# Kernel tuning notes

Hardware: AMD Instinct MI355X
Metric: run time of the kernel (lower is better)

The kernel has to match this reference:

```python
import jax, jax.numpy as jnp
import numpy as np

B, S, D = 4, 1024, 2048
N_HEADS, N_KV_HEADS = 32, 8
HEAD_DIM = D // N_HEADS          # 64
HALF = HEAD_DIM // 2             # 32
N_REP = N_HEADS // N_KV_HEADS    # 4


def setup_inputs() -> dict:
    key = jax.random.key(0)
    ks = jax.random.split(key, 6)
    # rotary tables: freqs_cis = exp(i * t * theta^( -2j/d )), real cos/sin halves
    inv_freq = 1.0 / (10000.0 ** (np.arange(0, HEAD_DIM, 2, dtype=np.float32) / HEAD_DIM))
    t = np.arange(S, dtype=np.float32)
    angles = np.outer(t, inv_freq)  # [S, HALF]
    return {
        "x": jax.random.normal(ks[0], (B, S, D), dtype=jnp.float32),
        "pos_cos": jnp.asarray(np.cos(angles), dtype=jnp.float32),
        "pos_sin": jnp.asarray(np.sin(angles), dtype=jnp.float32),
        "wq": jax.random.normal(ks[1], (D, N_HEADS * HEAD_DIM), dtype=jnp.float32) / np.sqrt(D),
        "wk": jax.random.normal(ks[2], (D, N_KV_HEADS * HEAD_DIM), dtype=jnp.float32) / np.sqrt(D),
        "wv": jax.random.normal(ks[3], (D, N_KV_HEADS * HEAD_DIM), dtype=jnp.float32) / np.sqrt(D),
        "wo": jax.random.normal(ks[4], (D, D), dtype=jnp.float32) / np.sqrt(D),
    }


def _apply_rotary(t, cos, sin):
    # t: [B, S, H, head_dim]; pairs of consecutive elements form complex numbers
    te = t[..., 0::2]  # real parts  [B,S,H,HALF]
    to = t[..., 1::2]  # imag parts
    c = cos[None, :, None, :]
    s = sin[None, :, None, :]
    re = te * c - to * s
    im = te * s + to * c
    return jnp.stack([re, im], axis=-1).reshape(t.shape)


def reference(x, pos_cos, pos_sin, wq, wk, wv, wo):
    b, s, d = x.shape
    xq = (x @ wq).reshape(b, s, N_HEADS, HEAD_DIM)
    xk = (x @ wk).reshape(b, s, N_KV_HEADS, HEAD_DIM)
    xv = (x @ wv).reshape(b, s, N_KV_HEADS, HEAD_DIM)
    xq = _apply_rotary(xq, pos_cos, pos_sin)
    xk = _apply_rotary(xk, pos_cos, pos_sin)
    # GQA: repeat kv heads (kv head h -> heads h*N_REP..h*N_REP+N_REP-1)
    xk = jnp.repeat(xk, N_REP, axis=2)
    xv = jnp.repeat(xv, N_REP, axis=2)
    scores = jnp.einsum("bqhd,bkhd->bhqk", xq, xk) / np.sqrt(HEAD_DIM).astype(np.float32)
    causal = jnp.triu(jnp.ones((s, s), dtype=bool), k=1)
    scores = jnp.where(causal[None, None], jnp.float32(-jnp.inf), scores)
    attn = jax.nn.softmax(scores.astype(jnp.float32), axis=-1).astype(x.dtype)
    out = jnp.einsum("bhqk,bkhd->bqhd", attn, xv).reshape(b, s, d)
    return out @ wo
```

## Files before the change

kernel.cpp:

```cpp
#include <hip/hip_runtime.h>
#include <hip/hip_bf16.h>


typedef __bf16 bf16x8 __attribute__((ext_vector_type(8)));
typedef float  f32x4  __attribute__((ext_vector_type(4)));

#define DEV static __device__ __forceinline__

DEV unsigned short f2bf(float f) {
  __hip_bfloat16 h = __float2bfloat16(f);
  unsigned short u;
  __builtin_memcpy(&u, &h, 2);
  return u;
}
DEV float bf2f(unsigned short u) {
  unsigned int ui = ((unsigned int)u) << 16;
  float f;
  __builtin_memcpy(&f, &ui, 4);
  return f;
}

typedef const unsigned int __attribute__((address_space(1)))* as1_u32cp;
typedef unsigned int __attribute__((address_space(3)))* as3_u32p;

DEV void load16_lds(const unsigned short* g, unsigned short* l) {
  __builtin_amdgcn_global_load_lds((as1_u32cp)(unsigned long long)g,
                                   (as3_u32p)(unsigned int)(unsigned long long)l,
                                   16, 0, 0);
}

DEV f32x4 mfma16x16(bf16x8 a, bf16x8 b, f32x4 c) {
  return __builtin_amdgcn_mfma_f32_16x16x32_bf16(a, b, c, 0, 0, 0);
}

__global__ __launch_bounds__(256) void k_convert_x(const float* __restrict__ x,
                                                   unsigned short* __restrict__ xb, int n) {
  int i = (blockIdx.x * 256 + threadIdx.x) * 4;
  if (i < n) {
    float4 v = *(const float4*)(x + i);
    ushort4 o;
    o.x = f2bf(v.x); o.y = f2bf(v.y); o.z = f2bf(v.z); o.w = f2bf(v.w);
    *(ushort4*)(xb + i) = o;
  }
}

__global__ __launch_bounds__(256) void k_transpose_w(const float* __restrict__ src,
                                                     unsigned short* __restrict__ dst, int N) {
  __shared__ float t[32][33];
  const int n0 = blockIdx.x * 32, k0 = blockIdx.y * 32;
  const int tx = threadIdx.x & 31, ty = threadIdx.x >> 5;
#pragma unroll
  for (int i = 0; i < 4; i++) {
    int k = k0 + ty + i * 8;
    t[ty + i * 8][tx] = src[(size_t)k * N + n0 + tx];
  }
  __syncthreads();
#pragma unroll
  for (int i = 0; i < 4; i++) {
    int n = n0 + ty + i * 8;
    dst[(size_t)n * 2048 + k0 + tx] = f2bf(t[tx][ty + i * 8]);
  }
}


DEV bf16x8 ldfrag(const unsigned short* base, int row, int colslot) {
  return *(const bf16x8*)&base[row * 64 + (((colslot) ^ (row & 7)) << 3)];
}

template <int OUTF32>
__global__ __launch_bounds__(512) void k_gemm8(const unsigned short* __restrict__ A,
                                               const unsigned short* __restrict__ Bt,
                                               void* __restrict__ Cp, int M, int N, int K) {
  __shared__ __align__(16) unsigned short As[2][16384];
  __shared__ __align__(16) unsigned short Bs[2][16384];
  const int nbx = N >> 8;
  const int nwg = gridDim.x;
  int wg = blockIdx.x;
  wg = (wg & 7) * (nwg >> 3) + (wg >> 3);
  const int bx = wg % nbx, by = wg / nbx;
  const int m0 = by << 8, n0 = bx << 8;
  const int tid = threadIdx.x;
  const int lane = tid & 63, wid = tid >> 6;
  const int wm = wid >> 2, wn = wid & 3;
  const int l15 = lane & 15, kg = lane >> 4;
  const int NT = K >> 6;

  const int rl = tid >> 3;
  const int gcol = (((tid & 7) ^ (rl & 7)) << 3);
  const unsigned short* Ag = &A[(size_t)(m0 + rl) * K + gcol];
  const unsigned short* Bg = &Bt[(size_t)(n0 + rl) * K + gcol];
  const int ldsb = wid * 8 * 64;

#define STAGE_TILE(buf, kt)                                                        \
  {                                                                                \
    const int _k0 = (kt) << 6;                                                     \
    _Pragma("unroll") for (int i = 0; i < 4; i++)                                  \
        load16_lds(&Ag[(size_t)(i * 64) * K + _k0], &As[buf][i * 64 * 64 + ldsb]); \
    _Pragma("unroll") for (int i = 0; i < 4; i++)                                  \
        load16_lds(&Bg[(size_t)(i * 64) * K + _k0], &Bs[buf][i * 64 * 64 + ldsb]); \
  }

  f32x4 acc[8][4] = {};

  STAGE_TILE(0, 0)
  STAGE_TILE(1, 1)
  asm volatile("s_waitcnt vmcnt(8)" ::: "memory");
  __builtin_amdgcn_s_barrier();

  for (int t = 0; t < NT; t++) {
    const unsigned short* at = As[t & 1];
    const unsigned short* bt = Bs[t & 1];
    bf16x8 af[4][2], bfr[2][2];

#pragma unroll
    for (int fm = 0; fm < 4; fm++)
#pragma unroll
      for (int kc = 0; kc < 2; kc++)
        af[fm][kc] = ldfrag(at, wm * 128 + fm * 16 + l15, kc * 4 + kg);
#pragma unroll
    for (int fn = 0; fn < 2; fn++)
#pragma unroll
      for (int kc = 0; kc < 2; kc++)
        bfr[fn][kc] = ldfrag(bt, wn * 64 + fn * 16 + l15, kc * 4 + kg);
    __builtin_amdgcn_s_barrier();
    __builtin_amdgcn_s_setprio(1);
#pragma unroll
    for (int fm = 0; fm < 4; fm++)
#pragma unroll
      for (int fn = 0; fn < 2; fn++)
#pragma unroll
        for (int kc = 0; kc < 2; kc++)
          acc[fm][fn] = mfma16x16(af[fm][kc], bfr[fn][kc], acc[fm][fn]);
    __builtin_amdgcn_s_setprio(0);
    __builtin_amdgcn_s_barrier();

#pragma unroll
    for (int fn = 0; fn < 2; fn++)
#pragma unroll
      for (int kc = 0; kc < 2; kc++)
        bfr[fn][kc] = ldfrag(bt, wn * 64 + (2 + fn) * 16 + l15, kc * 4 + kg);
    __builtin_amdgcn_s_barrier();
    __builtin_amdgcn_s_setprio(1);
#pragma unroll
    for (int fm = 0; fm < 4; fm++)
#pragma unroll
      for (int fn = 0; fn < 2; fn++)
#pragma unroll
        for (int kc = 0; kc < 2; kc++)
          acc[fm][2 + fn] = mfma16x16(af[fm][kc], bfr[fn][kc], acc[fm][2 + fn]);
    __builtin_amdgcn_s_setprio(0);
    __builtin_amdgcn_s_barrier();

#pragma unroll
    for (int fm = 0; fm < 4; fm++)
#pragma unroll
      for (int kc = 0; kc < 2; kc++)
        af[fm][kc] = ldfrag(at, wm * 128 + (4 + fm) * 16 + l15, kc * 4 + kg);
    __builtin_amdgcn_s_barrier();
    __builtin_amdgcn_s_setprio(1);
#pragma unroll
    for (int fm = 0; fm < 4; fm++)
#pragma unroll
      for (int fn = 0; fn < 2; fn++)
#pragma unroll
        for (int kc = 0; kc < 2; kc++)
          acc[4 + fm][2 + fn] = mfma16x16(af[fm][kc], bfr[fn][kc], acc[4 + fm][2 + fn]);
    __builtin_amdgcn_s_setprio(0);
    __builtin_amdgcn_s_barrier();

#pragma unroll
    for (int fn = 0; fn < 2; fn++)
#pragma unroll
      for (int kc = 0; kc < 2; kc++)
        bfr[fn][kc] = ldfrag(bt, wn * 64 + fn * 16 + l15, kc * 4 + kg);
    __builtin_amdgcn_s_barrier();
    __builtin_amdgcn_s_setprio(1);
#pragma unroll
    for (int fm = 0; fm < 4; fm++)
#pragma unroll
      for (int fn = 0; fn < 2; fn++)
#pragma unroll
        for (int kc = 0; kc < 2; kc++)
          acc[4 + fm][fn] = mfma16x16(af[fm][kc], bfr[fn][kc], acc[4 + fm][fn]);
    __builtin_amdgcn_s_setprio(0);
    __builtin_amdgcn_s_barrier();

    if (t + 2 < NT) {
      STAGE_TILE(t & 1, t + 2)
      asm volatile("s_waitcnt vmcnt(8)" ::: "memory");
    } else {
      asm volatile("s_waitcnt vmcnt(0)" ::: "memory");
    }
    __builtin_amdgcn_s_barrier();
  }
#undef STAGE_TILE

  const int orow = m0 + wm * 128 + kg * 4;
#pragma unroll
  for (int fm = 0; fm < 8; fm++) {
#pragma unroll
    for (int fn = 0; fn < 4; fn++) {
      const int col = n0 + wn * 64 + fn * 16 + l15;
#pragma unroll
      for (int j = 0; j < 4; j++) {
        const size_t off = (size_t)(orow + fm * 16 + j) * N + col;
        if (OUTF32)
          ((float*)Cp)[off] = acc[fm][fn][j];
        else
          ((unsigned short*)Cp)[off] = f2bf(acc[fm][fn][j]);
      }
    }
  }
}

__global__ __launch_bounds__(256) void k_rope(unsigned short* __restrict__ qkv,
                                              const float* __restrict__ ctab,
                                              const float* __restrict__ stab) {
  const int idx = blockIdx.x * 256 + threadIdx.x;
  const int row = idx / 1280;
  const int r = idx - row * 1280;
  const int head = r >> 5, pair = r & 31;
  const int s = row & 1023;
  const int col = (head < 32) ? (head * 64 + pair * 2) : (2048 + (head - 32) * 64 + pair * 2);
  const float c = ctab[s * 32 + pair], sn = stab[s * 32 + pair];
  const size_t base = (size_t)row * 3072 + col;
  const float e = bf2f(qkv[base]), o = bf2f(qkv[base + 1]);
  qkv[base]     = f2bf(e * c - o * sn);
  qkv[base + 1] = f2bf(e * sn + o * c);
}

__global__ __launch_bounds__(256) void k_vt(const unsigned short* __restrict__ qkv,
                                            unsigned short* __restrict__ vt) {
  __shared__ unsigned short t[32][33];
  const int st0 = blockIdx.x * 32;
  const int d0 = blockIdx.y * 32;
  const int bkh = blockIdx.z;
  const int b = bkh >> 3, kh = bkh & 7;
  const int tx = threadIdx.x & 31, ty = threadIdx.x >> 5;
#pragma unroll
  for (int i = 0; i < 4; i++) {
    int s = st0 + ty + i * 8;
    t[ty + i * 8][tx] = qkv[(size_t)(b * 1024 + s) * 3072 + 2560 + kh * 64 + d0 + tx];
  }
  __syncthreads();
#pragma unroll
  for (int i = 0; i < 4; i++) {
    int d = d0 + ty + i * 8;
    vt[(size_t)(bkh * 64 + d) * 1024 + st0 + tx] = t[tx][ty + i * 8];
  }
}

__global__ __launch_bounds__(256) void k_attn(const unsigned short* __restrict__ qkv,
                                              const unsigned short* __restrict__ vt,
                                              unsigned short* __restrict__ ao) {
  __shared__ __align__(16) unsigned short Ks[2][64 * 64];
  __shared__ __align__(16) unsigned short Vs[2][64 * 64];
  __shared__ __align__(16) unsigned short P[4][16][72];

  const int bid = blockIdx.x;
  const int qt = 15 - (bid >> 7);
  const int hb = bid & 127;
  const int h = hb & 31, b = hb >> 5;
  const int q0 = qt << 6;
  const int wid = threadIdx.x >> 6, lane = threadIdx.x & 63;
  const int l15 = lane & 15, kg = lane >> 4;
  const int kh = h >> 2;
  const int qbase = b * 1024 + q0 + wid * 16;
  const int nt = qt + 1;

  bf16x8 aq0, aq1;
  {
    const size_t qoff = (size_t)(qbase + l15) * 3072 + h * 64 + kg * 8;
    aq0 = *(const bf16x8*)&qkv[qoff];
    aq1 = *(const bf16x8*)&qkv[qoff + 32];
  }

  const int l8 = lane >> 3;
  const int colel = ((lane & 7) ^ l8) * 8;
  const size_t krowbase = (size_t)(b * 1024) * 3072 + 2048 + kh * 64 + colel;
  const size_t vrowbase = (size_t)((b * 8 + kh) * 64) * 1024 + colel;

#pragma unroll
  for (int i = 0; i < 2; i++) {
    const int r = wid * 16 + i * 8 + l8;
    load16_lds(&qkv[krowbase + (size_t)r * 3072], &Ks[0][(wid * 16 + i * 8) * 64]);
    load16_lds(&vt[vrowbase + (size_t)r * 1024], &Vs[0][(wid * 16 + i * 8) * 64]);
  }
  asm volatile("s_waitcnt vmcnt(0)" ::: "memory");
  __builtin_amdgcn_s_barrier();

  f32x4 o[4] = {};
  float mrow[4] = {-__builtin_inff(), -__builtin_inff(), -__builtin_inff(), -__builtin_inff()};
  float lrow[4] = {0.f, 0.f, 0.f, 0.f};

  const int swz = (l15 & 7) * 8;

  for (int t = 0; t < nt; t++) {
    const int cur = t & 1;
    if (t + 1 < nt) {
      const size_t kv1 = (size_t)((t + 1) << 6);
#pragma unroll
      for (int i = 0; i < 2; i++) {
        const int r = wid * 16 + i * 8 + l8;
        load16_lds(&qkv[krowbase + (kv1 + r) * 3072], &Ks[cur ^ 1][(wid * 16 + i * 8) * 64]);
        load16_lds(&vt[vrowbase + (size_t)r * 1024 + kv1], &Vs[cur ^ 1][(wid * 16 + i * 8) * 64]);
      }
    }
    const int kv0 = t << 6;

    f32x4 sc[4] = {};
#pragma unroll
    for (int ct = 0; ct < 4; ct++) {
      const unsigned short* kr = &Ks[cur][(ct * 16 + l15) * 64];
      bf16x8 bk0 = *(const bf16x8*)&kr[(kg * 8) ^ swz];
      bf16x8 bk1 = *(const bf16x8*)&kr[(kg * 8 + 32) ^ swz];
      sc[ct] = mfma16x16(aq0, bk0, sc[ct]);
      sc[ct] = mfma16x16(aq1, bk1, sc[ct]);
    }

    float pv[4][4];
    float fac[4];
#pragma unroll
    for (int reg = 0; reg < 4; reg++) {
      const int rowg = q0 + wid * 16 + kg * 4 + reg;
      float rm = -__builtin_inff();
#pragma unroll
      for (int ct = 0; ct < 4; ct++) {
        float v = sc[ct][reg] * 0.125f;
        const int colg = kv0 + ct * 16 + l15;
        v = (colg > rowg) ? -__builtin_inff() : v;
        pv[ct][reg] = v;
        rm = fmaxf(rm, v);
      }
#pragma unroll
      for (int off = 1; off < 16; off <<= 1) rm = fmaxf(rm, __shfl_xor(rm, off));
      const float mnew = fmaxf(mrow[reg], rm);
      fac[reg] = __expf(mrow[reg] - mnew);
      float rs = 0.f;
#pragma unroll
      for (int ct = 0; ct < 4; ct++) {
        const float e = __expf(pv[ct][reg] - mnew);
        pv[ct][reg] = e;
        rs += e;
      }
#pragma unroll
      for (int off = 1; off < 16; off <<= 1) rs += __shfl_xor(rs, off);
      lrow[reg] = lrow[reg] * fac[reg] + rs;
      mrow[reg] = mnew;
    }
#pragma unroll
    for (int ct = 0; ct < 4; ct++) {
      o[ct][0] *= fac[0]; o[ct][1] *= fac[1]; o[ct][2] *= fac[2]; o[ct][3] *= fac[3];
    }

#pragma unroll
    for (int reg = 0; reg < 4; reg++)
#pragma unroll
      for (int ct = 0; ct < 4; ct++)
        P[wid][kg * 4 + reg][ct * 16 + l15] = f2bf(pv[ct][reg]);

    bf16x8 ap0 = *(const bf16x8*)&P[wid][l15][kg * 8];
    bf16x8 ap1 = *(const bf16x8*)&P[wid][l15][32 + kg * 8];

#pragma unroll
    for (int ct = 0; ct < 4; ct++) {
      const unsigned short* vr = &Vs[cur][(ct * 16 + l15) * 64];
      bf16x8 bv0 = *(const bf16x8*)&vr[(kg * 8) ^ swz];
      bf16x8 bv1 = *(const bf16x8*)&vr[(kg * 8 + 32) ^ swz];
      o[ct] = mfma16x16(ap0, bv0, o[ct]);
      o[ct] = mfma16x16(ap1, bv1, o[ct]);
    }

    asm volatile("s_waitcnt vmcnt(0)" ::: "memory");
    __builtin_amdgcn_s_barrier();
  }

#pragma unroll
  for (int ct = 0; ct < 4; ct++) {
#pragma unroll
    for (int reg = 0; reg < 4; reg++) {
      const float val = o[ct][reg] / lrow[reg];
      ao[(size_t)(qbase + kg * 4 + reg) * 2048 + h * 64 + ct * 16 + l15] = f2bf(val);
    }
  }
}

extern "C" void kernel_launch(void* const* d_in, const int* in_sizes, int n_in,
                              void* d_out, int out_size, void* d_ws, size_t ws_size,
                              hipStream_t stream) {
  const float* x    = (const float*)d_in[0];
  const float* pcos = (const float*)d_in[1];
  const float* psin = (const float*)d_in[2];
  const float* wq   = (const float*)d_in[3];
  const float* wk   = (const float*)d_in[4];
  const float* wv   = (const float*)d_in[5];
  const float* wo   = (const float*)d_in[6];

  char* ws = (char*)d_ws;
  unsigned short* XB  = (unsigned short*)(ws);
  unsigned short* WT  = (unsigned short*)(ws + 16777216);
  unsigned short* WOT = (unsigned short*)(ws + 29360128);
  unsigned short* QKV = (unsigned short*)(ws + 37748736);
  unsigned short* VT  = (unsigned short*)(ws + 62914560);

  k_convert_x<<<8192, 256, 0, stream>>>(x, XB, 8388608);
  k_transpose_w<<<dim3(64, 64), 256, 0, stream>>>(wq, WT, 2048);
  k_transpose_w<<<dim3(16, 64), 256, 0, stream>>>(wk, WT + (size_t)2048 * 2048, 512);
  k_transpose_w<<<dim3(16, 64), 256, 0, stream>>>(wv, WT + (size_t)2560 * 2048, 512);
  k_transpose_w<<<dim3(64, 64), 256, 0, stream>>>(wo, WOT, 2048);

  k_gemm8<0><<<192, 512, 0, stream>>>(XB, WT, QKV, 4096, 3072, 2048);
  k_rope<<<20480, 256, 0, stream>>>(QKV, pcos, psin);
  k_vt<<<dim3(32, 2, 32), 256, 0, stream>>>(QKV, VT);
  k_attn<<<2048, 256, 0, stream>>>(QKV, VT, XB);
  k_gemm8<1><<<128, 512, 0, stream>>>(XB, WOT, d_out, 4096, 2048, 2048);
}
```

Measured before the change: 337.0 us.

## Restructure GEMM pipeline with 4-stage K=32 buffers and optimize attention softmax

The GEMM kernel is templated on tile shape and warp layout. It now uses a four-deep ring of K=32 half-tiles with interleaved prefetch and counted vmcnt waits, and the output projection uses 128-wide N tiles to launch more workgroups. The attention kernel folds the softmax scale and log2(e) into Q, switches to exp2, and applies the causal mask only on the diagonal tile. It also skips the rescale of the output accumulator when the running max grows by at most 8, and raises wave priority around the MFMAs. These target LDS and barrier stalls in the GEMMs and VALU work in the softmax. The trade-offs are more complex pipeline bookkeeping, extra bf16 rounding of the scaled Q, and a lazy max that could risk overflow in edge cases.

```diff
diff --git a/kernel.cpp b/kernel.cpp
--- a/kernel.cpp
+++ b/kernel.cpp
@@ -62,145 +62,139 @@
   }
 }
 
-
-DEV bf16x8 ldfrag(const unsigned short* base, int row, int colslot) {
-  return *(const bf16x8*)&base[row * 64 + (((colslot) ^ (row & 7)) << 3)];
-}
-
-template <int OUTF32>
+template <int OUTF32, int BN, int WM, int WN>
 __global__ __launch_bounds__(512) void k_gemm8(const unsigned short* __restrict__ A,
                                                const unsigned short* __restrict__ Bt,
                                                void* __restrict__ Cp, int M, int N, int K) {
-  __shared__ __align__(16) unsigned short As[2][16384];
-  __shared__ __align__(16) unsigned short Bs[2][16384];
-  const int nbx = N >> 8;
+  constexpr int BM = 256;
+  constexpr int FM = BM / WM / 16;
+  constexpr int FN = BN / WN / 16;
+  constexpr int LA = BM * 4 / 512;
+  constexpr int LB = BN * 4 / 512;
+  constexpr int LH = LA + LB;
+  __shared__ __align__(16) unsigned short As[4][BM * 32];
+  __shared__ __align__(16) unsigned short Bs[4][BN * 32];
+
+  const int nbx = N / BN;
   const int nwg = gridDim.x;
   int wg = blockIdx.x;
   wg = (wg & 7) * (nwg >> 3) + (wg >> 3);
   const int bx = wg % nbx, by = wg / nbx;
-  const int m0 = by << 8, n0 = bx << 8;
+  const int m0 = by << 8, n0 = bx * BN;
   const int tid = threadIdx.x;
   const int lane = tid & 63, wid = tid >> 6;
-  const int wm = wid >> 2, wn = wid & 3;
+  const int wm = wid / WN, wn = wid % WN;
   const int l15 = lane & 15, kg = lane >> 4;
+  const int H = K >> 5;
   const int NT = K >> 6;
 
-  const int rl = tid >> 3;
-  const int gcol = (((tid & 7) ^ (rl & 7)) << 3);
-  const unsigned short* Ag = &A[(size_t)(m0 + rl) * K + gcol];
-  const unsigned short* Bg = &Bt[(size_t)(n0 + rl) * K + gcol];
-  const int ldsb = wid * 8 * 64;
-
-#define STAGE_TILE(buf, kt)                                                        \
-  {                                                                                \
-    const int _k0 = (kt) << 6;                                                     \
-    _Pragma("unroll") for (int i = 0; i < 4; i++)                                  \
-        load16_lds(&Ag[(size_t)(i * 64) * K + _k0], &As[buf][i * 64 * 64 + ldsb]); \
-    _Pragma("unroll") for (int i = 0; i < 4; i++)                                  \
-        load16_lds(&Bg[(size_t)(i * 64) * K + _k0], &Bs[buf][i * 64 * 64 + ldsb]); \
-  }
-
-  f32x4 acc[8][4] = {};
-
-  STAGE_TILE(0, 0)
-  STAGE_TILE(1, 1)
-  asm volatile("s_waitcnt vmcnt(8)" ::: "memory");
+  auto stageA = [&](int h, int i) {
+    const int u = i * 512 + tid;
+    const int row = u >> 2, sl = u & 3;
+    const int gc = ((sl ^ ((row >> 1) & 3)) << 3);
+    load16_lds(&A[(size_t)(m0 + row) * K + (h << 5) + gc],
+               &As[h & 3][(i * 512 + (tid & ~63)) * 8]);
+  };
+  auto stageB = [&](int h, int i) {
+    const int u = i * 512 + tid;
+    const int row = u >> 2, sl = u & 3;
+    const int gc = ((sl ^ ((row >> 1) & 3)) << 3);
+    load16_lds(&Bt[(size_t)(n0 + row) * K + (h << 5) + gc],
+               &Bs[h & 3][(i * 512 + (tid & ~63)) * 8]);
+  };
+  auto lda = [&](int s, int r) {
+    return *(const bf16x8*)&As[s][r * 32 + ((kg ^ ((r >> 1) & 3)) << 3)];
+  };
+  auto ldb = [&](int s, int r) {
+    return *(const bf16x8*)&Bs[s][r * 32 + ((kg ^ ((r >> 1) & 3)) << 3)];
+  };
+
+#define VMCNT_C2(c)                                                   \
+  if ((c) == 2)      asm volatile("s_waitcnt vmcnt(%0)" ::"n"(2 * LH) : "memory"); \
+  else if ((c) == 1) asm volatile("s_waitcnt vmcnt(%0)" ::"n"(LH) : "memory");     \
+  else               asm volatile("s_waitcnt vmcnt(0)" ::: "memory");
+
+  const int rowA0 = wm * (BM / WM) + l15;
+  const int rowB0 = wn * (BN / WN) + l15;
+
+  bf16x8 af[FM / 2], bf[FN];
+  f32x4 acc[FM][FN] = {};
+
+#pragma unroll
+  for (int h = 0; h < 3; h++) {
+    stageA(h, 0); stageA(h, 1);
+    stageB(h, 0); if (LB > 1) stageB(h, 1);
+  }
+  asm volatile("s_waitcnt vmcnt(%0)" ::"n"(2 * LH) : "memory");
   __builtin_amdgcn_s_barrier();
 
   for (int t = 0; t < NT; t++) {
-    const unsigned short* at = As[t & 1];
-    const unsigned short* bt = Bs[t & 1];
-    bf16x8 af[4][2], bfr[2][2];
-
-#pragma unroll
-    for (int fm = 0; fm < 4; fm++)
-#pragma unroll
-      for (int kc = 0; kc < 2; kc++)
-        af[fm][kc] = ldfrag(at, wm * 128 + fm * 16 + l15, kc * 4 + kg);
-#pragma unroll
-    for (int fn = 0; fn < 2; fn++)
-#pragma unroll
-      for (int kc = 0; kc < 2; kc++)
-        bfr[fn][kc] = ldfrag(bt, wn * 64 + fn * 16 + l15, kc * 4 + kg);
-    __builtin_amdgcn_s_barrier();
-    __builtin_amdgcn_s_setprio(1);
-#pragma unroll
-    for (int fm = 0; fm < 4; fm++)
-#pragma unroll
-      for (int fn = 0; fn < 2; fn++)
-#pragma unroll
-        for (int kc = 0; kc < 2; kc++)
-          acc[fm][fn] = mfma16x16(af[fm][kc], bfr[fn][kc], acc[fm][fn]);
-    __builtin_amdgcn_s_setprio(0);
-    __builtin_amdgcn_s_barrier();
-
-#pragma unroll
-    for (int fn = 0; fn < 2; fn++)
-#pragma unroll
-      for (int kc = 0; kc < 2; kc++)
-        bfr[fn][kc] = ldfrag(bt, wn * 64 + (2 + fn) * 16 + l15, kc * 4 + kg);
-    __builtin_amdgcn_s_barrier();
-    __builtin_amdgcn_s_setprio(1);
-#pragma unroll
-    for (int fm = 0; fm < 4; fm++)
-#pragma unroll
-      for (int fn = 0; fn < 2; fn++)
-#pragma unroll
-        for (int kc = 0; kc < 2; kc++)
-          acc[fm][2 + fn] = mfma16x16(af[fm][kc], bfr[fn][kc], acc[fm][2 + fn]);
-    __builtin_amdgcn_s_setprio(0);
-    __builtin_amdgcn_s_barrier();
-
-#pragma unroll
-    for (int fm = 0; fm < 4; fm++)
-#pragma unroll
-      for (int kc = 0; kc < 2; kc++)
-        af[fm][kc] = ldfrag(at, wm * 128 + (4 + fm) * 16 + l15, kc * 4 + kg);
-    __builtin_amdgcn_s_barrier();
-    __builtin_amdgcn_s_setprio(1);
-#pragma unroll
-    for (int fm = 0; fm < 4; fm++)
-#pragma unroll
-      for (int fn = 0; fn < 2; fn++)
-#pragma unroll
-        for (int kc = 0; kc < 2; kc++)
-          acc[4 + fm][2 + fn] = mfma16x16(af[fm][kc], bfr[fn][kc], acc[4 + fm][2 + fn]);
-    __builtin_amdgcn_s_setprio(0);
-    __builtin_amdgcn_s_barrier();
-
-#pragma unroll
-    for (int fn = 0; fn < 2; fn++)
-#pragma unroll
-      for (int kc = 0; kc < 2; kc++)
-        bfr[fn][kc] = ldfrag(bt, wn * 64 + fn * 16 + l15, kc * 4 + kg);
-    __builtin_amdgcn_s_barrier();
-    __builtin_amdgcn_s_setprio(1);
-#pragma unroll
-    for (int fm = 0; fm < 4; fm++)
-#pragma unroll
-      for (int fn = 0; fn < 2; fn++)
-#pragma unroll
-        for (int kc = 0; kc < 2; kc++)
-          acc[4 + fm][fn] = mfma16x16(af[fm][kc], bfr[fn][kc], acc[4 + fm][fn]);
-    __builtin_amdgcn_s_setprio(0);
-    __builtin_amdgcn_s_barrier();
-
-    if (t + 2 < NT) {
-      STAGE_TILE(t & 1, t + 2)
-      asm volatile("s_waitcnt vmcnt(8)" ::: "memory");
-    } else {
-      asm volatile("s_waitcnt vmcnt(0)" ::: "memory");
-    }
-    __builtin_amdgcn_s_barrier();
-  }
-#undef STAGE_TILE
-
-  const int orow = m0 + wm * 128 + kg * 4;
-#pragma unroll
-  for (int fm = 0; fm < 8; fm++) {
-#pragma unroll
-    for (int fn = 0; fn < 4; fn++) {
-      const int col = n0 + wn * 64 + fn * 16 + l15;
+    const int s0 = (2 * t) & 3, s1 = (2 * t + 1) & 3;
+    const int h3 = 2 * t + 3, h4 = 2 * t + 4;
+    const bool v2 = (2 * t + 2) < H, v3 = h3 < H, v4 = h4 < H;
+
+#pragma unroll
+    for (int f = 0; f < FM / 2; f++) af[f] = lda(s0, rowA0 + f * 16);
+#pragma unroll
+    for (int g = 0; g < FN; g++) bf[g] = ldb(s0, rowB0 + g * 16);
+    if (v3) { stageA(h3, 0); stageA(h3, 1); }
+    __builtin_amdgcn_s_barrier();
+    __builtin_amdgcn_s_setprio(1);
+#pragma unroll
+    for (int f = 0; f < FM / 2; f++)
+#pragma unroll
+      for (int g = 0; g < FN; g++) acc[f][g] = mfma16x16(af[f], bf[g], acc[f][g]);
+    __builtin_amdgcn_s_setprio(0);
+
+#pragma unroll
+    for (int f = 0; f < FM / 2; f++) af[f] = lda(s0, rowA0 + (FM / 2 + f) * 16);
+    if (v3) { stageB(h3, 0); if (LB > 1) stageB(h3, 1); }
+    __builtin_amdgcn_s_barrier();
+    __builtin_amdgcn_s_setprio(1);
+#pragma unroll
+    for (int f = 0; f < FM / 2; f++)
+#pragma unroll
+      for (int g = 0; g < FN; g++)
+        acc[FM / 2 + f][g] = mfma16x16(af[f], bf[g], acc[FM / 2 + f][g]);
+    __builtin_amdgcn_s_setprio(0);
+    { const int c = (int)v2 + (int)v3; VMCNT_C2(c) }
+    __builtin_amdgcn_s_barrier();
+
+#pragma unroll
+    for (int f = 0; f < FM / 2; f++) af[f] = lda(s1, rowA0 + f * 16);
+#pragma unroll
+    for (int g = 0; g < FN; g++) bf[g] = ldb(s1, rowB0 + g * 16);
+    if (v4) { stageA(h4, 0); stageA(h4, 1); }
+    __builtin_amdgcn_s_barrier();
+    __builtin_amdgcn_s_setprio(1);
+#pragma unroll
+    for (int f = 0; f < FM / 2; f++)
+#pragma unroll
+      for (int g = 0; g < FN; g++) acc[f][g] = mfma16x16(af[f], bf[g], acc[f][g]);
+    __builtin_amdgcn_s_setprio(0);
+
+#pragma unroll
+    for (int f = 0; f < FM / 2; f++) af[f] = lda(s1, rowA0 + (FM / 2 + f) * 16);
+    if (v4) { stageB(h4, 0); if (LB > 1) stageB(h4, 1); }
+    __builtin_amdgcn_s_barrier();
+    __builtin_amdgcn_s_setprio(1);
+#pragma unroll
+    for (int f = 0; f < FM / 2; f++)
+#pragma unroll
+      for (int g = 0; g < FN; g++)
+        acc[FM / 2 + f][g] = mfma16x16(af[f], bf[g], acc[FM / 2 + f][g]);
+    __builtin_amdgcn_s_setprio(0);
+    { const int c = (int)v3 + (int)v4; VMCNT_C2(c) }
+    __builtin_amdgcn_s_barrier();
+  }
+#undef VMCNT_C2
+
+  const int orow = m0 + wm * (BM / WM) + kg * 4;
+#pragma unroll
+  for (int fm = 0; fm < FM; fm++) {
+#pragma unroll
+    for (int fn = 0; fn < FN; fn++) {
+      const int col = n0 + wn * (BN / WN) + fn * 16 + l15;
 #pragma unroll
       for (int j = 0; j < 4; j++) {
         const size_t off = (size_t)(orow + fm * 16 + j) * N + col;
@@ -267,12 +261,18 @@
   const int kh = h >> 2;
   const int qbase = b * 1024 + q0 + wid * 16;
   const int nt = qt + 1;
+  const float NEGINF = -__builtin_inff();
 
   bf16x8 aq0, aq1;
   {
     const size_t qoff = (size_t)(qbase + l15) * 3072 + h * 64 + kg * 8;
     aq0 = *(const bf16x8*)&qkv[qoff];
     aq1 = *(const bf16x8*)&qkv[qoff + 32];
+#pragma unroll
+    for (int i = 0; i < 8; i++) {
+      aq0[i] = (__bf16)((float)aq0[i] * 0.18033688011112042f);
+      aq1[i] = (__bf16)((float)aq1[i] * 0.18033688011112042f);
+    }
   }
 
   const int l8 = lane >> 3;
@@ -290,7 +290,7 @@
   __builtin_amdgcn_s_barrier();
 
   f32x4 o[4] = {};
-  float mrow[4] = {-__builtin_inff(), -__builtin_inff(), -__builtin_inff(), -__builtin_inff()};
+  float mrow[4] = {NEGINF, NEGINF, NEGINF, NEGINF};
   float lrow[4] = {0.f, 0.f, 0.f, 0.f};
 
   const int swz = (l15 & 7) * 8;
@@ -309,6 +309,7 @@
     const int kv0 = t << 6;
 
     f32x4 sc[4] = {};
+    __builtin_amdgcn_s_setprio(1);
 #pragma unroll
     for (int ct = 0; ct < 4; ct++) {
       const unsigned short* kr = &Ks[cur][(ct * 16 + l15) * 64];
@@ -317,51 +318,85 @@
       sc[ct] = mfma16x16(aq0, bk0, sc[ct]);
       sc[ct] = mfma16x16(aq1, bk1, sc[ct]);
     }
-
-    float pv[4][4];
-    float fac[4];
+    __builtin_amdgcn_s_setprio(0);
+
+    float p[4][4];
+    if (t == qt) {
+#pragma unroll
+      for (int reg = 0; reg < 4; reg++) {
+        const int rowg = q0 + wid * 16 + kg * 4 + reg;
+#pragma unroll
+        for (int ct = 0; ct < 4; ct++) {
+          const int colg = kv0 + ct * 16 + l15;
+          p[ct][reg] = (colg > rowg) ? NEGINF : sc[ct][reg];
+        }
+      }
+    } else {
+#pragma unroll
+      for (int reg = 0; reg < 4; reg++)
+#pragma unroll
+        for (int ct = 0; ct < 4; ct++) p[ct][reg] = sc[ct][reg];
+    }
+
+    float rm[4];
 #pragma unroll
     for (int reg = 0; reg < 4; reg++) {
-      const int rowg = q0 + wid * 16 + kg * 4 + reg;
-      float rm = -__builtin_inff();
+      float v = fmaxf(fmaxf(p[0][reg], p[1][reg]), fmaxf(p[2][reg], p[3][reg]));
+#pragma unroll
+      for (int off = 1; off < 16; off <<= 1) v = fmaxf(v, __shfl_xor(v, off));
+      rm[reg] = v;
+    }
+
+    const int okl = (rm[0] <= mrow[0] + 8.f) && (rm[1] <= mrow[1] + 8.f) &&
+                    (rm[2] <= mrow[2] + 8.f) && (rm[3] <= mrow[3] + 8.f);
+    if (__all(okl)) {
+#pragma unroll
+      for (int reg = 0; reg < 4; reg++) {
+        float rs = 0.f;
+#pragma unroll
+        for (int ct = 0; ct < 4; ct++) {
+          const float e = exp2f(p[ct][reg] - mrow[reg]);
+          p[ct][reg] = e;
+          rs += e;
+        }
+#pragma unroll
+        for (int off = 1; off < 16; off <<= 1) rs += __shfl_xor(rs, off);
+        lrow[reg] += rs;
+      }
+    } else {
+      float fac[4];
+#pragma unroll
+      for (int reg = 0; reg < 4; reg++) {
+        const float mnew = fmaxf(mrow[reg], rm[reg]);
+        fac[reg] = exp2f(mrow[reg] - mnew);
+        float rs = 0.f;
+#pragma unroll
+        for (int ct = 0; ct < 4; ct++) {
+          const float e = exp2f(p[ct][reg] - mnew);
+          p[ct][reg] = e;
+          rs += e;
+        }
+#pragma unroll
+        for (int off = 1; off < 16; off <<= 1) rs += __shfl_xor(rs, off);
+        lrow[reg] = lrow[reg] * fac[reg] + rs;
+        mrow[reg] = mnew;
+      }
 #pragma unroll
       for (int ct = 0; ct < 4; ct++) {
-        float v = sc[ct][reg] * 0.125f;
-        const int colg = kv0 + ct * 16 + l15;
-        v = (colg > rowg) ? -__builtin_inff() : v;
-        pv[ct][reg] = v;
-        rm = fmaxf(rm, v);
-      }
-#pragma unroll
-      for (int off = 1; off < 16; off <<= 1) rm = fmaxf(rm, __shfl_xor(rm, off));
-      const float mnew = fmaxf(mrow[reg], rm);
-      fac[reg] = __expf(mrow[reg] - mnew);
-      float rs = 0.f;
-#pragma unroll
-      for (int ct = 0; ct < 4; ct++) {
-        const float e = __expf(pv[ct][reg] - mnew);
-        pv[ct][reg] = e;
-        rs += e;
-      }
-#pragma unroll
-      for (int off = 1; off < 16; off <<= 1) rs += __shfl_xor(rs, off);
-      lrow[reg] = lrow[reg] * fac[reg] + rs;
-      mrow[reg] = mnew;
-    }
-#pragma unroll
-    for (int ct = 0; ct < 4; ct++) {
-      o[ct][0] *= fac[0]; o[ct][1] *= fac[1]; o[ct][2] *= fac[2]; o[ct][3] *= fac[3];
+        o[ct][0] *= fac[0]; o[ct][1] *= fac[1]; o[ct][2] *= fac[2]; o[ct][3] *= fac[3];
+      }
     }
 
 #pragma unroll
     for (int reg = 0; reg < 4; reg++)
 #pragma unroll
       for (int ct = 0; ct < 4; ct++)
-        P[wid][kg * 4 + reg][ct * 16 + l15] = f2bf(pv[ct][reg]);
+        P[wid][kg * 4 + reg][ct * 16 + l15] = f2bf(p[ct][reg]);
 
     bf16x8 ap0 = *(const bf16x8*)&P[wid][l15][kg * 8];
     bf16x8 ap1 = *(const bf16x8*)&P[wid][l15][32 + kg * 8];
 
+    __builtin_amdgcn_s_setprio(1);
 #pragma unroll
     for (int ct = 0; ct < 4; ct++) {
       const unsigned short* vr = &Vs[cur][(ct * 16 + l15) * 64];
@@ -370,6 +405,7 @@
       o[ct] = mfma16x16(ap0, bv0, o[ct]);
       o[ct] = mfma16x16(ap1, bv1, o[ct]);
     }
+    __builtin_amdgcn_s_setprio(0);
 
     asm volatile("s_waitcnt vmcnt(0)" ::: "memory");
     __builtin_amdgcn_s_barrier();
@@ -409,9 +445,9 @@
   k_transpose_w<<<dim3(16, 64), 256, 0, stream>>>(wv, WT + (size_t)2560 * 2048, 512);
   k_transpose_w<<<dim3(64, 64), 256, 0, stream>>>(wo, WOT, 2048);
 
-  k_gemm8<0><<<192, 512, 0, stream>>>(XB, WT, QKV, 4096, 3072, 2048);
+  k_gemm8<0, 256, 2, 4><<<192, 512, 0, stream>>>(XB, WT, QKV, 4096, 3072, 2048);
   k_rope<<<20480, 256, 0, stream>>>(QKV, pcos, psin);
   k_vt<<<dim3(32, 2, 32), 256, 0, stream>>>(QKV, VT);
   k_attn<<<2048, 256, 0, stream>>>(QKV, VT, XB);
-  k_gemm8<1><<<128, 512, 0, stream>>>(XB, WOT, d_out, 4096, 2048, 2048);
-}
+  k_gemm8<1, 128, 4, 2><<<256, 512, 0, stream>>>(XB, WOT, d_out, 4096, 2048, 2048);
+}
```

After: 302.3 us. 1.11x faster.
